# Kernel tuning notes

Measured on AMD Instinct MI355X. Metric: run time of the kernel, lower is better.

## Reference

```python
import jax, jax.numpy as jnp
import numpy as np

B, N, HIST, PRED = 32, 4096, 16, 8
IN_DIM, HID, GCN_OUT, E = 10, 32, 2, 65536


def setup_inputs() -> dict:
    key = jax.random.key(0)
    ks = jax.random.split(key, 11)
    s = 0.15  # keep gate pre-activations in a sane range
    return {
        "pm25_hist": jax.random.normal(ks[0], (B, HIST, N), jnp.float32),
        "feature": jax.random.normal(ks[1], (B, HIST + PRED, N, IN_DIM - 1), jnp.float32),
        "edge_index": jax.random.randint(ks[2], (2, E), 0, N, dtype=jnp.int32),
        "cheb_w": jax.random.normal(ks[3], (2, IN_DIM, GCN_OUT), jnp.float32) * s,
        "cheb_b": jax.random.normal(ks[4], (GCN_OUT,), jnp.float32) * s,
        "x2h_w": jax.random.normal(ks[5], (IN_DIM + GCN_OUT, 4 * HID), jnp.float32) * s,
        "x2h_b": jax.random.normal(ks[6], (4 * HID,), jnp.float32) * s,
        "h2h_w": jax.random.normal(ks[7], (HID, 4 * HID), jnp.float32) * s,
        "h2h_b": jax.random.normal(ks[8], (4 * HID,), jnp.float32) * s,
        "fc_w": jax.random.normal(ks[9], (HID, 1), jnp.float32) * s,
        "fc_b": jax.random.normal(ks[10], (1,), jnp.float32) * s,
    }


def _cheb_norm(edge_index):
    # PyG ChebConv(K=2, sym norm, lambda_max=2): Tx1 = -D^{-1/2} A D^{-1/2} x, zero diagonal
    src, dst = edge_index[0], edge_index[1]
    deg = jnp.zeros((N,), jnp.float32).at[src].add(1.0)
    dis = jnp.where(deg > 0, jax.lax.rsqrt(jnp.maximum(deg, 1e-12)), 0.0)
    return -dis[src] * dis[dst], src, dst


def _cheb_conv(x, src, dst, norm, W, b):
    # x: [B,N,F]; message x[src] aggregated at dst
    msg = x[:, src, :] * norm[None, :, None]
    tx1 = jnp.zeros_like(x[..., :1].repeat(x.shape[-1], -1)).at[:, dst, :].add(msg)
    return jnp.einsum("bnf,fo->bno", x, W[0]) + jnp.einsum("bnf,fo->bno", tx1, W[1]) + b


def _lstm(x, h, c, x2h_w, x2h_b, h2h_w, h2h_b):
    g = x @ x2h_w + x2h_b + h @ h2h_w + h2h_b  # [B,N,4H]
    i, f, gc, o = jnp.split(g, 4, axis=-1)
    c = jax.nn.sigmoid(f) * c + jax.nn.sigmoid(i) * jnp.tanh(gc)
    h = jax.nn.sigmoid(o) * jnp.tanh(c)
    return h, c


def reference(pm25_hist, feature, edge_index, cheb_w, cheb_b, x2h_w, x2h_b, h2h_w, h2h_b, fc_w, fc_b):
    norm, src, dst = _cheb_norm(edge_index)

    def step(carry, x):
        h, c = carry
        xg = jax.nn.sigmoid(_cheb_conv(x, src, dst, norm, cheb_w, cheb_b))
        h, c = _lstm(jnp.concatenate([x, xg], -1), h, c, x2h_w, x2h_b, h2h_w, h2h_b)
        return (h, c), None

    h = jnp.zeros((B, N, HID), jnp.float32)
    c = jnp.zeros((B, N, HID), jnp.float32)

    # history phase
    xs_hist = jnp.concatenate([pm25_hist[..., None], feature[:, :HIST]], -1)  # [B,HIST,N,10]
    (h, c), _ = jax.lax.scan(step, (h, c), jnp.swapaxes(xs_hist, 0, 1))
    xn = h @ fc_w + fc_b  # [B,N,1]

    # prediction phase (recurrent through xn)
    def pred_step(carry, feat_t):
        h, c, xn = carry
        x = jnp.concatenate([xn, feat_t], -1)  # [B,N,10]
        (h, c), _ = step((h, c), x)
        xn = h @ fc_w + fc_b
        return (h, c, xn), xn

    _, ys = jax.lax.scan(pred_step, (h, c, xn), jnp.swapaxes(feature[:, HIST:], 0, 1))
    return jnp.squeeze(jnp.swapaxes(ys, 0, 1), -1)  # [B,PRED,N]
```

## Files before the change

### kernel.cpp

```cpp
#include <hip/hip_runtime.h>
#include <math.h>

#define Bb    32
#define Nn    4096
#define HISTC 16
#define PREDC 8
#define TTC   24
#define EC    65536
#define BN    (Bb*Nn)
#define NSL   768

typedef float f32x2 __attribute__((ext_vector_type(2)));
typedef float f32x4 __attribute__((ext_vector_type(4)));
typedef __fp16 f16x8 __attribute__((ext_vector_type(8)));
typedef __fp16 fp16v2 __attribute__((ext_vector_type(2)));

__device__ __forceinline__ float sigm_f(float x){
  return __builtin_amdgcn_rcpf(1.f + __expf(-x));
}
__device__ __forceinline__ float tanh_f(float x){
  return fmaf(-2.f, __builtin_amdgcn_rcpf(1.f + __expf(2.f*x)), 1.f);
}
__device__ __forceinline__ unsigned pk2(float a, float b){
  fp16v2 v = __builtin_amdgcn_cvt_pkrtz(a, b);
  return __builtin_bit_cast(unsigned, v);
}
__device__ __forceinline__ f32x4 mfma16(uint4 a, uint4 b, f32x4 c){
  return __builtin_amdgcn_mfma_f32_16x16x32_f16(
      __builtin_bit_cast(f16x8, a), __builtin_bit_cast(f16x8, b), c, 0, 0, 0);
}

__global__ void k_deg(const int* __restrict__ ei, int* deg, int* cnt){
  int e = blockIdx.x*blockDim.x + threadIdx.x;
  if (e < EC){ atomicAdd(&deg[ei[e]],1); atomicAdd(&cnt[ei[EC+e]],1); }
}
__global__ void k_dis(const int* __restrict__ deg, float* dis){
  int n = blockIdx.x*blockDim.x + threadIdx.x;
  if (n < Nn) dis[n] = deg[n] > 0 ? rsqrtf((float)deg[n]) : 0.f;
}
__global__ void k_scan(const int* __restrict__ cnt, int* ptr){
  __shared__ int sd[1024];
  int t = threadIdx.x;
  int c0=cnt[4*t], c1=cnt[4*t+1], c2=cnt[4*t+2], c3=cnt[4*t+3];
  int s = c0+c1+c2+c3;
  sd[t] = s; __syncthreads();
  for (int off=1; off<1024; off<<=1){
    int v = (t>=off) ? sd[t-off] : 0;
    __syncthreads();
    sd[t] += v;
    __syncthreads();
  }
  int excl = sd[t]-s;
  ptr[4*t]=excl; ptr[4*t+1]=excl+c0; ptr[4*t+2]=excl+c0+c1; ptr[4*t+3]=excl+c0+c1+c2;
  if (t==1023) ptr[4096]=sd[1023];
}
__global__ void k_fill(const int* __restrict__ ei, const float* __restrict__ dis,
                       const int* __restrict__ ptr, int* fillc, int2* __restrict__ epack){
  int e = blockIdx.x*blockDim.x + threadIdx.x;
  if (e < EC){
    int s = ei[e], d = ei[EC+e];
    int pos = ptr[d] + atomicAdd(&fillc[d],1);
    epack[pos] = make_int2(s, __float_as_int(-dis[s]*dis[d]));
  }
}

__global__ void k_prep(const float* __restrict__ x2hw, const float* __restrict__ h2hw,
                       const float* __restrict__ x2hb, const float* __restrict__ h2hb,
                       _Float16* __restrict__ wfrag){
  int i = blockIdx.x*256 + threadIdx.x;
  int f = i >> 9, lane = (i >> 3) & 63, j = i & 7;
  int kt = f >> 3, ct = f & 7;
  int k = kt*32 + (lane>>4)*8 + j;
  int col = ct*16 + (lane&15);
  float v;
  if (k < 12)       v = x2hw[k*128 + col];
  else if (k == 12) v = x2hb[col] + h2hb[col];
  else if (k < 32)  v = 0.f;
  else              v = h2hw[(k-32)*128 + col];
  wfrag[f*512 + lane*8 + j] = (_Float16)v;
}

__global__ __launch_bounds__(256)
void k_zh(const float* __restrict__ pm25, const float* __restrict__ feat,
          const float* __restrict__ cw, f32x2* __restrict__ zAll){
  int r = blockIdx.x*256 + threadIdx.x;
  int t = r >> 17, bn = r & (BN-1);
  int b = bn >> 12, n = bn & (Nn-1);
  const float* fp = feat + ((size_t)(b*TTC + t)*Nn + n)*9;
  float x[10];
  x[0] = pm25[(size_t)(b*HISTC + t)*Nn + n];
  #pragma unroll
  for (int f=0;f<9;++f) x[1+f] = fp[f];
  float z0=0.f, z1=0.f;
  #pragma unroll
  for (int f=0;f<10;++f){
    z0 += x[f]*cw[20+f*2+0]; z1 += x[f]*cw[20+f*2+1];
  }
  zAll[((size_t)(t*Bb + b))*Nn + n] = (f32x2){z0, z1};
}

__global__ __launch_bounds__(256)
void k_zf(const float* __restrict__ feat, const float* __restrict__ cw,
          f32x2* __restrict__ zAll){
  int r = blockIdx.x*256 + threadIdx.x;
  int tp = r >> 17, bn = r & (BN-1);
  int b = bn >> 12, n = bn & (Nn-1);
  int t = HISTC + tp;
  const float* fp = feat + ((size_t)(b*TTC + t)*Nn + n)*9;
  float z0=0.f, z1=0.f;
  #pragma unroll
  for (int f=0;f<9;++f){
    float v = fp[f];
    z0 += v*cw[20+(f+1)*2+0]; z1 += v*cw[20+(f+1)*2+1];
  }
  zAll[((size_t)(512 + tp*Bb + b))*Nn + n] = (f32x2){z0, z1};
}

__global__ __launch_bounds__(256)
void k_tr(const f32x2* __restrict__ in, f32x2* __restrict__ out, int R, int C){
  __shared__ f32x2 tile[64][65];
  int tilesR = R >> 6;
  int br = blockIdx.x % tilesR, bc = blockIdx.x / tilesR;
  int r0 = br << 6, c0 = bc << 6;
  for (int i=threadIdx.x; i<4096; i+=256){
    int r = i>>6, c = i&63;
    tile[r][c] = in[(size_t)(r0+r)*C + c0+c];
  }
  __syncthreads();
  for (int i=threadIdx.x; i<4096; i+=256){
    int r = i>>6, c = i&63;
    out[(size_t)(c0+r)*R + r0+c] = tile[c][r];
  }
}

__global__ __launch_bounds__(64)
void k_aggc(const int* __restrict__ ptr, const int2* __restrict__ epack,
            const float4* __restrict__ zT, float4* __restrict__ aggT){
  int n  = blockIdx.x & (Nn-1);
  int cb = blockIdx.x >> 12;
  int col = cb*64 + threadIdx.x;
  int p0 = ptr[n], p1 = ptr[n+1];
  f32x4 acc = {0.f,0.f,0.f,0.f};
  int i = p0;
  for (; i+1 < p1; i += 2){
    int2 e0 = epack[i], e1 = epack[i+1];
    float w0 = __int_as_float(e0.y), w1 = __int_as_float(e1.y);
    float4 z0 = zT[(size_t)e0.x*384 + col];
    float4 z1 = zT[(size_t)e1.x*384 + col];
    acc.x = fmaf(w0, z0.x, acc.x); acc.y = fmaf(w0, z0.y, acc.y);
    acc.z = fmaf(w0, z0.z, acc.z); acc.w = fmaf(w0, z0.w, acc.w);
    acc.x = fmaf(w1, z1.x, acc.x); acc.y = fmaf(w1, z1.y, acc.y);
    acc.z = fmaf(w1, z1.z, acc.z); acc.w = fmaf(w1, z1.w, acc.w);
  }
  if (i < p1){
    int2 e = epack[i];
    float w = __int_as_float(e.y);
    float4 z = zT[(size_t)e.x*384 + col];
    acc.x = fmaf(w, z.x, acc.x); acc.y = fmaf(w, z.y, acc.y);
    acc.z = fmaf(w, z.z, acc.z); acc.w = fmaf(w, z.w, acc.w);
  }
  aggT[(size_t)n*384 + col] = make_float4(acc.x, acc.y, acc.z, acc.w);
}

__global__ __launch_bounds__(256)
void k_aggx(const int* __restrict__ ptr, const int2* __restrict__ epack,
            const float* __restrict__ xnT, float* __restrict__ aggx){
  int lane = threadIdx.x & 63, w = threadIdx.x >> 6;
  int n = blockIdx.x*4 + w;
  int b = lane & 31, half = lane >> 5;
  int p0 = ptr[n], p1 = ptr[n+1];
  float acc = 0.f;
  for (int i = p0 + half; i < p1; i += 2){
    int2 e = epack[i];
    acc = fmaf(__int_as_float(e.y), xnT[(size_t)e.x*32 + b], acc);
  }
  acc += __shfl_xor(acc, 32);
  if (lane < 32) aggx[(size_t)b*Nn + n] = acc;
}

#define POINTWISE(r)                                                            \
  c0[r] = fmaf(sigm_f(acc[0][r]), tanh_f(acc[4][r]), sigm_f(acc[2][r])*c0[r]);  \
  h0[r] = sigm_f(acc[6][r])*tanh_f(c0[r]);                                      \
  c1[r] = fmaf(sigm_f(acc[1][r]), tanh_f(acc[5][r]), sigm_f(acc[3][r])*c1[r]);  \
  h1[r] = sigm_f(acc[7][r])*tanh_f(c1[r]);

__global__ __launch_bounds__(256,1)
void k_hist(const float* __restrict__ pm25, const float* __restrict__ feat,
            const f32x2* __restrict__ aggH,
            const float* __restrict__ cw, const float* __restrict__ cb,
            const uint4* __restrict__ wfrag,
            const float* __restrict__ fcw, const float* __restrict__ fcb,
            uint4* __restrict__ hfragO, float4* __restrict__ cO,
            float* __restrict__ xn0, float* __restrict__ xnT){
  __shared__ __align__(16) uint4 wl[1024];
  __shared__ __align__(16) _Float16 hl[4][16][40];
  int tid = threadIdx.x;
  int lane = tid & 63, w = tid >> 6;
  for (int i = tid; i < 1024; i += 256) wl[i] = wfrag[i];
  int gw = blockIdx.x*4 + w;
  int r0 = gw*16;
  int b = r0 >> 12, n0 = r0 & (Nn-1);
  int l15 = lane & 15, g4 = lane >> 4;
  int nrow = n0 + l15;
  const float* pb = pm25 + (size_t)b*HISTC*Nn + nrow;
  const float* fb = feat + ((size_t)b*TTC*Nn + nrow)*9;

  float fw0 = fcw[l15], fw1 = fcw[l15+16];
  const f32x4 zacc = {0.f,0.f,0.f,0.f};

  uint4 ah = make_uint4(0,0,0,0);
  float c0[4]={0,0,0,0}, c1[4]={0,0,0,0};
  float h0[4], h1[4];
  __syncthreads();

  #pragma unroll 1
  for (int t=0; t<HISTC; ++t){
    int wofs = lane;
    asm volatile("" : "+v"(wofs));
    const float* fbt = fb + (size_t)t*Nn*9;
    float xv[9]; float a0 = 0.f, a1 = 0.f; float x0 = 0.f;
    if (g4 == 0){
      x0 = pb[(size_t)t*Nn];
      #pragma unroll
      for (int f=0;f<7;++f) xv[f] = fbt[f];
      a0 = x0*cw[0]; a1 = x0*cw[1];
      #pragma unroll
      for (int f=0;f<7;++f){ a0 += xv[f]*cw[(f+1)*2]; a1 += xv[f]*cw[(f+1)*2+1]; }
    } else if (g4 == 1){
      xv[7] = fbt[7]; xv[8] = fbt[8];
      a0 = cb[0] + xv[7]*cw[16] + xv[8]*cw[18];
      a1 = cb[1] + xv[7]*cw[17] + xv[8]*cw[19];
    } else if (g4 == 2){
      f32x2 ag = aggH[((size_t)(t*Bb + b))*Nn + nrow];
      a0 = ag.x; a1 = ag.y;
    }
    a0 += __shfl_xor(a0, 16); a0 += __shfl_xor(a0, 32);
    a1 += __shfl_xor(a1, 16); a1 += __shfl_xor(a1, 32);
    float xg0 = sigm_f(a0), xg1 = sigm_f(a1);

    uint4 ax;
    if (g4 == 0){
      ax.x = pk2(x0, xv[0]);     ax.y = pk2(xv[1], xv[2]);
      ax.z = pk2(xv[3], xv[4]);  ax.w = pk2(xv[5], xv[6]);
    } else if (g4 == 1){
      ax.x = pk2(xv[7], xv[8]);  ax.y = pk2(xg0, xg1);
      ax.z = pk2(1.f, 0.f);      ax.w = 0u;
    } else {
      ax = make_uint4(0,0,0,0);
    }

    f32x4 acc[8];
    #pragma unroll
    for (int ct=0; ct<8; ++ct){
      uint4 b0 = wl[wofs + ct*64];
      uint4 b1 = wl[wofs + 512 + ct*64];
      acc[ct] = mfma16(ax, b0, zacc);
      acc[ct] = mfma16(ah, b1, acc[ct]);
    }

    POINTWISE(0) POINTWISE(1) POINTWISE(2) POINTWISE(3)

    #pragma unroll
    for (int r=0;r<4;++r){
      hl[w][g4*4+r][l15]    = (_Float16)h0[r];
      hl[w][g4*4+r][l15+16] = (_Float16)h1[r];
    }
    asm volatile("s_waitcnt lgkmcnt(0)" ::: "memory");
    ah = *(const uint4*)&hl[w][l15][g4*8];
  }

  hfragO[(size_t)gw*64 + lane] = ah;
  cO[((size_t)gw*64 + lane)*2]   = make_float4(c0[0],c0[1],c0[2],c0[3]);
  cO[((size_t)gw*64 + lane)*2+1] = make_float4(c1[0],c1[1],c1[2],c1[3]);
  #pragma unroll
  for (int r=0;r<4;++r){
    float p = fmaf(h0[r], fw0, h1[r]*fw1);
    p += __shfl_xor(p, 1, 16); p += __shfl_xor(p, 2, 16);
    p += __shfl_xor(p, 4, 16); p += __shfl_xor(p, 8, 16);
    if (l15 == 0){
      float rr = p + fcb[0];
      int nr = n0 + g4*4 + r;
      xn0[r0 + g4*4 + r] = rr;
      xnT[(size_t)nr*32 + b] = rr;
    }
  }
}

__global__ __launch_bounds__(256,1)
void k_pred_cell(const float* __restrict__ feat, float* __restrict__ xn0,
                 const f32x2* __restrict__ aggzf,
                 const float* __restrict__ aggx,
                 const float* __restrict__ cw, const float* __restrict__ cb,
                 const uint4* __restrict__ wfrag,
                 const float* __restrict__ fcw, const float* __restrict__ fcb,
                 uint4* __restrict__ hfrag, float4* __restrict__ cS,
                 float* __restrict__ xnT, float* __restrict__ out, int t){
  __shared__ __align__(16) uint4 wl[1024];
  __shared__ __align__(16) _Float16 hl[4][16][40];
  int tid = threadIdx.x;
  int lane = tid & 63, w = tid >> 6;
  for (int i = tid; i < 1024; i += 256) wl[i] = wfrag[i];
  int gw = blockIdx.x*4 + w;
  int r0 = gw*16;
  int b = r0 >> 12, n0 = r0 & (Nn-1);
  int l15 = lane & 15, g4 = lane >> 4;
  int nrow = n0 + l15;

  float fw0 = fcw[l15], fw1 = fcw[l15+16];

  uint4 ah = hfrag[(size_t)gw*64 + lane];
  float4 cv0 = cS[((size_t)gw*64 + lane)*2];
  float4 cv1 = cS[((size_t)gw*64 + lane)*2+1];
  float c0[4] = {cv0.x, cv0.y, cv0.z, cv0.w};
  float c1[4] = {cv1.x, cv1.y, cv1.z, cv1.w};
  float h0[4], h1[4];
  const f32x4 zacc = {0.f,0.f,0.f,0.f};

  const float* fbt = feat + ((size_t)(b*TTC + t)*Nn + nrow)*9;
  float xv[9]; float a0 = 0.f, a1 = 0.f; float x0 = 0.f;
  if (g4 == 0){
    x0 = xn0[r0 + l15];
    #pragma unroll
    for (int f=0;f<7;++f) xv[f] = fbt[f];
    a0 = x0*cw[0]; a1 = x0*cw[1];
    #pragma unroll
    for (int f=0;f<7;++f){ a0 += xv[f]*cw[(f+1)*2]; a1 += xv[f]*cw[(f+1)*2+1]; }
  } else if (g4 == 1){
    xv[7] = fbt[7]; xv[8] = fbt[8];
    a0 = cb[0] + xv[7]*cw[16] + xv[8]*cw[18];
    a1 = cb[1] + xv[7]*cw[17] + xv[8]*cw[19];
  } else if (g4 == 2){
    f32x2 azf = aggzf[(size_t)b*Nn + nrow];
    float axv = aggx[(size_t)b*Nn + nrow];
    a0 = fmaf(cw[20], axv, azf.x);
    a1 = fmaf(cw[21], axv, azf.y);
  }
  a0 += __shfl_xor(a0, 16); a0 += __shfl_xor(a0, 32);
  a1 += __shfl_xor(a1, 16); a1 += __shfl_xor(a1, 32);
  float xg0 = sigm_f(a0), xg1 = sigm_f(a1);

  uint4 ax;
  if (g4 == 0){
    ax.x = pk2(x0, xv[0]);     ax.y = pk2(xv[1], xv[2]);
    ax.z = pk2(xv[3], xv[4]);  ax.w = pk2(xv[5], xv[6]);
  } else if (g4 == 1){
    ax.x = pk2(xv[7], xv[8]);  ax.y = pk2(xg0, xg1);
    ax.z = pk2(1.f, 0.f);      ax.w = 0u;
  } else {
    ax = make_uint4(0,0,0,0);
  }

  __syncthreads();
  f32x4 acc[8];
  #pragma unroll
  for (int ct=0; ct<8; ++ct){
    uint4 b0 = wl[lane + ct*64];
    uint4 b1 = wl[lane + 512 + ct*64];
    acc[ct] = mfma16(ax, b0, zacc);
    acc[ct] = mfma16(ah, b1, acc[ct]);
  }

  POINTWISE(0) POINTWISE(1) POINTWISE(2) POINTWISE(3)

  #pragma unroll
  for (int r=0;r<4;++r){
    hl[w][g4*4+r][l15]    = (_Float16)h0[r];
    hl[w][g4*4+r][l15+16] = (_Float16)h1[r];
  }
  asm volatile("s_waitcnt lgkmcnt(0)" ::: "memory");
  ah = *(const uint4*)&hl[w][l15][g4*8];

  hfrag[(size_t)gw*64 + lane] = ah;
  cS[((size_t)gw*64 + lane)*2]   = make_float4(c0[0],c0[1],c0[2],c0[3]);
  cS[((size_t)gw*64 + lane)*2+1] = make_float4(c1[0],c1[1],c1[2],c1[3]);
  #pragma unroll
  for (int r=0;r<4;++r){
    float p = fmaf(h0[r], fw0, h1[r]*fw1);
    p += __shfl_xor(p, 1, 16); p += __shfl_xor(p, 2, 16);
    p += __shfl_xor(p, 4, 16); p += __shfl_xor(p, 8, 16);
    if (l15 == 0){
      float rr = p + fcb[0];
      int nr = n0 + g4*4 + r;
      xn0[r0 + g4*4 + r] = rr;
      xnT[(size_t)nr*32 + b] = rr;
      out[(size_t)b*PREDC*Nn + nr] = rr;
    }
  }
}

extern "C" void kernel_launch(void* const* d_in, const int* in_sizes, int n_in,
                              void* d_out, int out_size, void* d_ws, size_t ws_size,
                              hipStream_t stream){
  const float* pm25 = (const float*)d_in[0];
  const float* feat = (const float*)d_in[1];
  const int*   ei   = (const int*)d_in[2];
  const float* cw   = (const float*)d_in[3];
  const float* cb   = (const float*)d_in[4];
  const float* x2hw = (const float*)d_in[5];
  const float* x2hb = (const float*)d_in[6];
  const float* h2hw = (const float*)d_in[7];
  const float* h2hb = (const float*)d_in[8];
  const float* fcw  = (const float*)d_in[9];
  const float* fcb  = (const float*)d_in[10];
  float* out = (float*)d_out;

  char* wsp = (char*)d_ws;
  size_t off = 0;
  auto take = [&](size_t bytes)->char*{
    char* r = wsp + off; off += (bytes + 255) & ~(size_t)255; return r;
  };
  int*      deg   = (int*)      take(Nn*4);
  int*      cnt   = (int*)      take(Nn*4);
  int*      fillc = (int*)      take(Nn*4);
  int*      ptr   = (int*)      take((Nn+1)*4);
  float*    dis   = (float*)    take(Nn*4);
  int2*     epack = (int2*)     take(EC*8);
  _Float16* wfrag = (_Float16*) take(16*512*2);
  char*     bufA  =             take((size_t)NSL*Nn*8);
  char*     bufB  =             take((size_t)NSL*Nn*8);
  float*    xn0   = (float*)    take((size_t)BN*4);
  float*    xnT   = (float*)    take((size_t)BN*4);
  float*    aggx  = (float*)    take((size_t)BN*4);

  f32x2* zAll = (f32x2*)bufA;
  f32x2* zT   = (f32x2*)bufB;
  uint4*  hfrag = (uint4*)bufA;
  float4* cbuf  = (float4*)(bufA + (size_t)8388608);

  (void)hipMemsetAsync(deg, 0, Nn*4*3, stream);

  k_deg <<<EC/256, 256, 0, stream>>>(ei, deg, cnt);
  k_dis <<<Nn/256, 256, 0, stream>>>(deg, dis);
  k_scan<<<1, 1024, 0, stream>>>(cnt, ptr);
  k_fill<<<EC/256, 256, 0, stream>>>(ei, dis, ptr, fillc, epack);
  k_prep<<<32, 256, 0, stream>>>(x2hw, h2hw, x2hb, h2hb, wfrag);

  k_zh<<<(HISTC*BN)/256, 256, 0, stream>>>(pm25, feat, cw, zAll);
  k_zf<<<(PREDC*BN)/256, 256, 0, stream>>>(feat, cw, zAll);
  k_tr<<<(NSL/64)*(Nn/64), 256, 0, stream>>>(zAll, zT, NSL, Nn);
  k_aggc<<<6*Nn, 64, 0, stream>>>(ptr, epack, (const float4*)zT, (float4*)zAll);
  k_tr<<<(Nn/64)*(NSL/64), 256, 0, stream>>>((const f32x2*)zAll, (f32x2*)bufB, Nn, NSL);

  const f32x2* aggAll = (const f32x2*)bufB;

  k_hist<<<BN/64, 256, 0, stream>>>(pm25, feat, aggAll, cw, cb,
                                    (const uint4*)wfrag, fcw, fcb,
                                    hfrag, cbuf, xn0, xnT);

  for (int tp = 0; tp < PREDC; ++tp){
    int t = HISTC + tp;
    k_aggx<<<Nn/4, 256, 0, stream>>>(ptr, epack, xnT, aggx);
    k_pred_cell<<<BN/64, 256, 0, stream>>>(feat, xn0,
                                           aggAll + (size_t)(512 + tp*Bb)*Nn, aggx,
                                           cw, cb, (const uint4*)wfrag, fcw, fcb,
                                           hfrag, cbuf, xnT, out + (size_t)tp*Nn, t);
  }
}
```

Measured before the change: 404.7 us.

## Merge setup kernels, fuse LSTM gate transcendentals, store cell state in fp16

Folds k_dis and k_prep into one k_misc launch and k_zh and k_zf into one k_zall launch, which cuts launch count. The LSTM pointwise math is rewritten to combine the sigmoid and tanh terms over shared denominators, so each cell needs fewer reciprocals. The cell state written between the history and prediction kernels is packed to fp16, halving that traffic. The fp16 cell state across eight recurrent steps adds precision loss, and the clamped exponentials change numerics slightly.

```diff
diff --git a/kernel.cpp b/kernel.cpp
--- a/kernel.cpp
+++ b/kernel.cpp
@@ -18,13 +18,14 @@
 __device__ __forceinline__ float sigm_f(float x){
   return __builtin_amdgcn_rcpf(1.f + __expf(-x));
 }
-__device__ __forceinline__ float tanh_f(float x){
-  return fmaf(-2.f, __builtin_amdgcn_rcpf(1.f + __expf(2.f*x)), 1.f);
-}
 __device__ __forceinline__ unsigned pk2(float a, float b){
   fp16v2 v = __builtin_amdgcn_cvt_pkrtz(a, b);
   return __builtin_bit_cast(unsigned, v);
 }
+__device__ __forceinline__ void unpk2(unsigned u, float& a, float& b){
+  fp16v2 v = __builtin_bit_cast(fp16v2, u);
+  a = (float)v.x; b = (float)v.y;
+}
 __device__ __forceinline__ f32x4 mfma16(uint4 a, uint4 b, f32x4 c){
   return __builtin_amdgcn_mfma_f32_16x16x32_f16(
       __builtin_bit_cast(f16x8, a), __builtin_bit_cast(f16x8, b), c, 0, 0, 0);
@@ -33,10 +34,6 @@
 __global__ void k_deg(const int* __restrict__ ei, int* deg, int* cnt){
   int e = blockIdx.x*blockDim.x + threadIdx.x;
   if (e < EC){ atomicAdd(&deg[ei[e]],1); atomicAdd(&cnt[ei[EC+e]],1); }
-}
-__global__ void k_dis(const int* __restrict__ deg, float* dis){
-  int n = blockIdx.x*blockDim.x + threadIdx.x;
-  if (n < Nn) dis[n] = deg[n] > 0 ? rsqrtf((float)deg[n]) : 0.f;
 }
 __global__ void k_scan(const int* __restrict__ cnt, int* ptr){
   __shared__ int sd[1024];
@@ -54,6 +51,30 @@
   ptr[4*t]=excl; ptr[4*t+1]=excl+c0; ptr[4*t+2]=excl+c0+c1; ptr[4*t+3]=excl+c0+c1+c2;
   if (t==1023) ptr[4096]=sd[1023];
 }
+__global__ void k_misc(const int* __restrict__ deg, float* __restrict__ dis,
+                       const float* __restrict__ x2hw, const float* __restrict__ h2hw,
+                       const float* __restrict__ x2hb, const float* __restrict__ h2hb,
+                       _Float16* __restrict__ wfrag){
+  if (blockIdx.x == 0){
+    #pragma unroll
+    for (int k=0;k<4;++k){
+      int n = threadIdx.x + k*1024;
+      dis[n] = deg[n] > 0 ? rsqrtf((float)deg[n]) : 0.f;
+    }
+  } else {
+    int i = (blockIdx.x-1)*1024 + threadIdx.x;
+    int f = i >> 9, lane = (i >> 3) & 63, j = i & 7;
+    int kt = f >> 3, ct = f & 7;
+    int k = kt*32 + (lane>>4)*8 + j;
+    int col = ct*16 + (lane&15);
+    float v;
+    if (k < 12)       v = x2hw[k*128 + col];
+    else if (k == 12) v = x2hb[col] + h2hb[col];
+    else if (k < 32)  v = 0.f;
+    else              v = h2hw[(k-32)*128 + col];
+    wfrag[f*512 + lane*8 + j] = (_Float16)v;
+  }
+}
 __global__ void k_fill(const int* __restrict__ ei, const float* __restrict__ dis,
                        const int* __restrict__ ptr, int* fillc, int2* __restrict__ epack){
   int e = blockIdx.x*blockDim.x + threadIdx.x;
@@ -64,56 +85,33 @@
   }
 }
 
-__global__ void k_prep(const float* __restrict__ x2hw, const float* __restrict__ h2hw,
-                       const float* __restrict__ x2hb, const float* __restrict__ h2hb,
-                       _Float16* __restrict__ wfrag){
-  int i = blockIdx.x*256 + threadIdx.x;
-  int f = i >> 9, lane = (i >> 3) & 63, j = i & 7;
-  int kt = f >> 3, ct = f & 7;
-  int k = kt*32 + (lane>>4)*8 + j;
-  int col = ct*16 + (lane&15);
-  float v;
-  if (k < 12)       v = x2hw[k*128 + col];
-  else if (k == 12) v = x2hb[col] + h2hb[col];
-  else if (k < 32)  v = 0.f;
-  else              v = h2hw[(k-32)*128 + col];
-  wfrag[f*512 + lane*8 + j] = (_Float16)v;
-}
-
 __global__ __launch_bounds__(256)
-void k_zh(const float* __restrict__ pm25, const float* __restrict__ feat,
-          const float* __restrict__ cw, f32x2* __restrict__ zAll){
+void k_zall(const float* __restrict__ pm25, const float* __restrict__ feat,
+            const float* __restrict__ cw, f32x2* __restrict__ zAll){
   int r = blockIdx.x*256 + threadIdx.x;
-  int t = r >> 17, bn = r & (BN-1);
+  int ts = r >> 17, bn = r & (BN-1);
   int b = bn >> 12, n = bn & (Nn-1);
-  const float* fp = feat + ((size_t)(b*TTC + t)*Nn + n)*9;
-  float x[10];
-  x[0] = pm25[(size_t)(b*HISTC + t)*Nn + n];
-  #pragma unroll
-  for (int f=0;f<9;++f) x[1+f] = fp[f];
+  const float* fp = feat + ((size_t)(b*TTC + ts)*Nn + n)*9;
   float z0=0.f, z1=0.f;
-  #pragma unroll
-  for (int f=0;f<10;++f){
-    z0 += x[f]*cw[20+f*2+0]; z1 += x[f]*cw[20+f*2+1];
-  }
-  zAll[((size_t)(t*Bb + b))*Nn + n] = (f32x2){z0, z1};
-}
-
-__global__ __launch_bounds__(256)
-void k_zf(const float* __restrict__ feat, const float* __restrict__ cw,
-          f32x2* __restrict__ zAll){
-  int r = blockIdx.x*256 + threadIdx.x;
-  int tp = r >> 17, bn = r & (BN-1);
-  int b = bn >> 12, n = bn & (Nn-1);
-  int t = HISTC + tp;
-  const float* fp = feat + ((size_t)(b*TTC + t)*Nn + n)*9;
-  float z0=0.f, z1=0.f;
-  #pragma unroll
-  for (int f=0;f<9;++f){
-    float v = fp[f];
-    z0 += v*cw[20+(f+1)*2+0]; z1 += v*cw[20+(f+1)*2+1];
-  }
-  zAll[((size_t)(512 + tp*Bb + b))*Nn + n] = (f32x2){z0, z1};
+  int slice;
+  if (ts < HISTC){
+    float x0 = pm25[(size_t)(b*HISTC + ts)*Nn + n];
+    z0 = x0*cw[20]; z1 = x0*cw[21];
+    #pragma unroll
+    for (int f=0;f<9;++f){
+      float v = fp[f];
+      z0 = fmaf(v, cw[20+(f+1)*2+0], z0); z1 = fmaf(v, cw[20+(f+1)*2+1], z1);
+    }
+    slice = ts*Bb + b;
+  } else {
+    #pragma unroll
+    for (int f=0;f<9;++f){
+      float v = fp[f];
+      z0 = fmaf(v, cw[20+(f+1)*2+0], z0); z1 = fmaf(v, cw[20+(f+1)*2+1], z1);
+    }
+    slice = 512 + (ts-HISTC)*Bb + b;
+  }
+  zAll[(size_t)slice*Nn + n] = (f32x2){z0, z1};
 }
 
 __global__ __launch_bounds__(256)
@@ -178,11 +176,23 @@
   if (lane < 32) aggx[(size_t)b*Nn + n] = acc;
 }
 
-#define POINTWISE(r)                                                            \
-  c0[r] = fmaf(sigm_f(acc[0][r]), tanh_f(acc[4][r]), sigm_f(acc[2][r])*c0[r]);  \
-  h0[r] = sigm_f(acc[6][r])*tanh_f(c0[r]);                                      \
-  c1[r] = fmaf(sigm_f(acc[1][r]), tanh_f(acc[5][r]), sigm_f(acc[3][r])*c1[r]);  \
-  h1[r] = sigm_f(acc[7][r])*tanh_f(c1[r]);
+#define PW(r)                                                                     \
+  {                                                                               \
+    float Ei0=__expf(fmaxf(-acc[0][r],-30.f)), Ef0=__expf(fmaxf(-acc[2][r],-30.f));\
+    float Eg0=__expf(fminf(2.f*acc[4][r],60.f)), Eo0=__expf(fmaxf(-acc[6][r],-30.f));\
+    float di0=1.f+Ei0, df0=1.f+Ef0, dg0=1.f+Eg0;                                  \
+    float nu0=fmaf(c0[r]*di0, dg0, (Eg0-1.f)*df0);                                \
+    c0[r]=nu0*__builtin_amdgcn_rcpf(di0*df0*dg0);                                 \
+    float Ec0=__expf(2.f*c0[r]);                                                  \
+    h0[r]=(Ec0-1.f)*__builtin_amdgcn_rcpf((Ec0+1.f)*(1.f+Eo0));                   \
+    float Ei1=__expf(fmaxf(-acc[1][r],-30.f)), Ef1=__expf(fmaxf(-acc[3][r],-30.f));\
+    float Eg1=__expf(fminf(2.f*acc[5][r],60.f)), Eo1=__expf(fmaxf(-acc[7][r],-30.f));\
+    float di1=1.f+Ei1, df1=1.f+Ef1, dg1=1.f+Eg1;                                  \
+    float nu1=fmaf(c1[r]*di1, dg1, (Eg1-1.f)*df1);                                \
+    c1[r]=nu1*__builtin_amdgcn_rcpf(di1*df1*dg1);                                 \
+    float Ec1=__expf(2.f*c1[r]);                                                  \
+    h1[r]=(Ec1-1.f)*__builtin_amdgcn_rcpf((Ec1+1.f)*(1.f+Eo1));                   \
+  }
 
 __global__ __launch_bounds__(256,1)
 void k_hist(const float* __restrict__ pm25, const float* __restrict__ feat,
@@ -190,7 +200,7 @@
             const float* __restrict__ cw, const float* __restrict__ cb,
             const uint4* __restrict__ wfrag,
             const float* __restrict__ fcw, const float* __restrict__ fcb,
-            uint4* __restrict__ hfragO, float4* __restrict__ cO,
+            uint4* __restrict__ hfragO, uint4* __restrict__ cO,
             float* __restrict__ xn0, float* __restrict__ xnT){
   __shared__ __align__(16) uint4 wl[1024];
   __shared__ __align__(16) _Float16 hl[4][16][40];
@@ -258,7 +268,7 @@
       acc[ct] = mfma16(ah, b1, acc[ct]);
     }
 
-    POINTWISE(0) POINTWISE(1) POINTWISE(2) POINTWISE(3)
+    PW(0) PW(1) PW(2) PW(3)
 
     #pragma unroll
     for (int r=0;r<4;++r){
@@ -270,8 +280,12 @@
   }
 
   hfragO[(size_t)gw*64 + lane] = ah;
-  cO[((size_t)gw*64 + lane)*2]   = make_float4(c0[0],c0[1],c0[2],c0[3]);
-  cO[((size_t)gw*64 + lane)*2+1] = make_float4(c1[0],c1[1],c1[2],c1[3]);
+  {
+    uint4 cp;
+    cp.x = pk2(c0[0], c0[1]); cp.y = pk2(c0[2], c0[3]);
+    cp.z = pk2(c1[0], c1[1]); cp.w = pk2(c1[2], c1[3]);
+    cO[(size_t)gw*64 + lane] = cp;
+  }
   #pragma unroll
   for (int r=0;r<4;++r){
     float p = fmaf(h0[r], fw0, h1[r]*fw1);
@@ -293,7 +307,7 @@
                  const float* __restrict__ cw, const float* __restrict__ cb,
                  const uint4* __restrict__ wfrag,
                  const float* __restrict__ fcw, const float* __restrict__ fcb,
-                 uint4* __restrict__ hfrag, float4* __restrict__ cS,
+                 uint4* __restrict__ hfrag, uint4* __restrict__ cS,
                  float* __restrict__ xnT, float* __restrict__ out, int t){
   __shared__ __align__(16) uint4 wl[1024];
   __shared__ __align__(16) _Float16 hl[4][16][40];
@@ -309,10 +323,12 @@
   float fw0 = fcw[l15], fw1 = fcw[l15+16];
 
   uint4 ah = hfrag[(size_t)gw*64 + lane];
-  float4 cv0 = cS[((size_t)gw*64 + lane)*2];
-  float4 cv1 = cS[((size_t)gw*64 + lane)*2+1];
-  float c0[4] = {cv0.x, cv0.y, cv0.z, cv0.w};
-  float c1[4] = {cv1.x, cv1.y, cv1.z, cv1.w};
+  float c0[4], c1[4];
+  {
+    uint4 cv = cS[(size_t)gw*64 + lane];
+    unpk2(cv.x, c0[0], c0[1]); unpk2(cv.y, c0[2], c0[3]);
+    unpk2(cv.z, c1[0], c1[1]); unpk2(cv.w, c1[2], c1[3]);
+  }
   float h0[4], h1[4];
   const f32x4 zacc = {0.f,0.f,0.f,0.f};
 
@@ -360,7 +376,7 @@
     acc[ct] = mfma16(ah, b1, acc[ct]);
   }
 
-  POINTWISE(0) POINTWISE(1) POINTWISE(2) POINTWISE(3)
+  PW(0) PW(1) PW(2) PW(3)
 
   #pragma unroll
   for (int r=0;r<4;++r){
@@ -371,8 +387,12 @@
   ah = *(const uint4*)&hl[w][l15][g4*8];
 
   hfrag[(size_t)gw*64 + lane] = ah;
-  cS[((size_t)gw*64 + lane)*2]   = make_float4(c0[0],c0[1],c0[2],c0[3]);
-  cS[((size_t)gw*64 + lane)*2+1] = make_float4(c1[0],c1[1],c1[2],c1[3]);
+  {
+    uint4 cp;
+    cp.x = pk2(c0[0], c0[1]); cp.y = pk2(c0[2], c0[3]);
+    cp.z = pk2(c1[0], c1[1]); cp.w = pk2(c1[2], c1[3]);
+    cS[(size_t)gw*64 + lane] = cp;
+  }
   #pragma unroll
   for (int r=0;r<4;++r){
     float p = fmaf(h0[r], fw0, h1[r]*fw1);
@@ -425,18 +445,16 @@
   f32x2* zAll = (f32x2*)bufA;
   f32x2* zT   = (f32x2*)bufB;
   uint4*  hfrag = (uint4*)bufA;
-  float4* cbuf  = (float4*)(bufA + (size_t)8388608);
+  uint4*  cbuf  = (uint4*)(bufA + (size_t)8388608);
 
   (void)hipMemsetAsync(deg, 0, Nn*4*3, stream);
 
   k_deg <<<EC/256, 256, 0, stream>>>(ei, deg, cnt);
-  k_dis <<<Nn/256, 256, 0, stream>>>(deg, dis);
   k_scan<<<1, 1024, 0, stream>>>(cnt, ptr);
+  k_misc<<<9, 1024, 0, stream>>>(deg, dis, x2hw, h2hw, x2hb, h2hb, wfrag);
   k_fill<<<EC/256, 256, 0, stream>>>(ei, dis, ptr, fillc, epack);
-  k_prep<<<32, 256, 0, stream>>>(x2hw, h2hw, x2hb, h2hb, wfrag);
-
-  k_zh<<<(HISTC*BN)/256, 256, 0, stream>>>(pm25, feat, cw, zAll);
-  k_zf<<<(PREDC*BN)/256, 256, 0, stream>>>(feat, cw, zAll);
+
+  k_zall<<<(TTC*BN)/256, 256, 0, stream>>>(pm25, feat, cw, zAll);
   k_tr<<<(NSL/64)*(Nn/64), 256, 0, stream>>>(zAll, zT, NSL, Nn);
   k_aggc<<<6*Nn, 64, 0, stream>>>(ptr, epack, (const float4*)zT, (float4*)zAll);
   k_tr<<<(Nn/64)*(NSL/64), 256, 0, stream>>>((const f32x2*)zAll, (f32x2*)bufB, Nn, NSL);
```

Measured after the change: 405.0 us. About the same (+0.1%).
